# Kernel tuning notes

Measured on AMD Instinct MI355X. Metric: run time of the kernel, lower is better.

The kernel has to match this reference:

```python
import jax, jax.numpy as jnp
import numpy as np

EPS = 1e-5

def _layernorm(x, g, b):
    mu = jnp.mean(x, axis=-1, keepdims=True)
    var = jnp.mean(jnp.square(x - mu), axis=-1, keepdims=True)
    return (x - mu) * jax.lax.rsqrt(var + EPS) * g + b

def setup_inputs() -> dict:
    key = jax.random.key(0)
    ks = jax.random.split(key, 12)
    B, S, D, F = 2, 2048, 1024, 4096
    w = lambda k, shp: jax.random.normal(k, shp, dtype=jnp.float32) * 0.02
    return {
        "x":  jax.random.normal(ks[0], (B, S, D), dtype=jnp.float32),
        "Wq": w(ks[1], (D, D)), "bq": jnp.zeros((D,), jnp.float32),
        "Wk": w(ks[2], (D, D)), "bk": jnp.zeros((D,), jnp.float32),
        "Wv": w(ks[3], (D, D)), "bv": jnp.zeros((D,), jnp.float32),
        "W1": w(ks[4], (F, D)), "b1": jnp.zeros((F,), jnp.float32),
        "W2": w(ks[5], (D, F)), "b2": jnp.zeros((D,), jnp.float32),
        "g1": jnp.ones((D,), jnp.float32), "beta1": jnp.zeros((D,), jnp.float32),
        "g2": jnp.ones((D,), jnp.float32), "beta2": jnp.zeros((D,), jnp.float32),
    }

def reference(x, Wq, bq, Wk, bk, Wv, bv, W1, b1, W2, b2, g1, beta1, g2, beta2):
    B, S, D = x.shape
    H = 16
    dk = D // H
    # QKV projections (torch nn.Linear: y = x @ W.T + b)
    q = (x @ Wq.T + bq).reshape(B, S, H, dk).transpose(0, 2, 1, 3)  # [B,H,S,dk]
    k = (x @ Wk.T + bk).reshape(B, S, H, dk).transpose(0, 2, 1, 3)
    v = (x @ Wv.T + bv).reshape(B, S, H, dk).transpose(0, 2, 1, 3)
    # naive full attention (no mask, dropout=identity in eval)
    scores = jnp.einsum("bhqd,bhkd->bhqk", q, k) / jnp.sqrt(jnp.float32(dk))
    probs = jax.nn.softmax(scores, axis=-1)
    attn = jnp.einsum("bhqk,bhkd->bhqd", probs, v)  # [B,H,S,dk]
    attn_out = attn.transpose(0, 2, 1, 3).reshape(B, S, D)  # NOTE: no output proj (combine unused in source)
    # residual + LN1
    h = _layernorm(x + attn_out, g1, beta1)
    # FFN: linear2(relu(linear1(h)))
    ffn = jax.nn.relu(h @ W1.T + b1) @ W2.T + b2
    # residual + LN2
    return _layernorm(h + ffn, g2, beta2)
```

## Files before the change

kernel.cpp:

```cpp
#include <hip/hip_runtime.h>
#include <stdint.h>

typedef unsigned short u16;
typedef __bf16 bf16x8 __attribute__((ext_vector_type(8)));
typedef short s16x8 __attribute__((ext_vector_type(8)));
typedef float f32x4 __attribute__((ext_vector_type(4)));

union FragU { s16x8 s; bf16x8 b; uint4 u; };

__device__ __forceinline__ f32x4 mfma_bf16(s16x8 a, s16x8 b, f32x4 c) {
    FragU ua, ub; ua.s = a; ub.s = b;
    return __builtin_amdgcn_mfma_f32_16x16x32_bf16(ua.b, ub.b, c, 0, 0, 0);
}

__device__ __forceinline__ u16 f2bf(float f) {
    uint32_t u = __float_as_uint(f);
    u += 0x7fffu + ((u >> 16) & 1u);
    return (u16)(u >> 16);
}

__device__ __forceinline__ float bf2f(u16 u) {
    return __uint_as_float((uint32_t)u << 16);
}

__device__ __forceinline__ void gload_lds16(const void* g, void* l) {
    __builtin_amdgcn_global_load_lds((__attribute__((address_space(1))) void*)g,
                                     (__attribute__((address_space(3))) void*)l,
                                     16, 0, 0);
}

__device__ __forceinline__ void xcd_swz(int& bx, int& by, int& bz) {
    int nx = gridDim.x, ny = gridDim.y;
    int nwg = nx * ny * gridDim.z;
    int lin = blockIdx.x + nx * (blockIdx.y + ny * blockIdx.z);
    int cpx = nwg >> 3;
    int s = (lin & 7) * cpx + (lin >> 3);
    bx = s % nx; s /= nx;
    by = s % ny; bz = s / ny;
}

__global__ void k_cast(const float* __restrict__ in, u16* __restrict__ out, int n4) {
    int i = blockIdx.x * blockDim.x + threadIdx.x;
    int stride = gridDim.x * blockDim.x;
    for (; i < n4; i += stride) {
        float4 v = ((const float4*)in)[i];
        u16 us[4] = {f2bf(v.x), f2bf(v.y), f2bf(v.z), f2bf(v.w)};
        *(uint2*)(out + (size_t)i * 4) = *(uint2*)us;
    }
}

template<int RELU, int OUTMODE>
__device__ __forceinline__ void gemm_body(
    u16* __restrict__ As, u16* __restrict__ Bs,
    const u16* __restrict__ A, const u16* __restrict__ W,
    const float* __restrict__ bias, void* __restrict__ Cout,
    int M, int N, int K, int row0, int col0, int kbeg, int kend)
{
    const int tid  = threadIdx.x;
    const int wid  = tid >> 6;
    const int lane = tid & 63;
    const int g    = lane >> 4;
    const int cc   = lane & 15;
    const int wr   = wid >> 1;
    const int wc   = wid & 1;

    f32x4 zero = {0.f, 0.f, 0.f, 0.f};
    f32x4 acc[4][4];
#pragma unroll
    for (int i = 0; i < 4; i++)
#pragma unroll
        for (int j = 0; j < 4; j++) acc[i][j] = zero;

    const int srow = tid >> 3;
    const int scol = ((tid & 7) ^ (srow & 7)) * 8;
    const u16* gA0 = A + (size_t)(row0 + srow) * K + scol;
    const u16* gB0 = W + (size_t)(col0 + srow) * K + scol;
    u16* lA0 = &As[wid * 512];
    u16* lB0 = &Bs[wid * 512];

    const int xm = (cc & 7);

    for (int k0 = kbeg; k0 < kend; k0 += 64) {
#pragma unroll
        for (int j = 0; j < 4; j++)
            gload_lds16(gA0 + (size_t)(j * 32) * K + k0, lA0 + j * 2048);
#pragma unroll
        for (int j = 0; j < 4; j++)
            gload_lds16(gB0 + (size_t)(j * 32) * K + k0, lB0 + j * 2048);
        __syncthreads();

#pragma unroll
        for (int h = 0; h < 2; h++) {
            const int slot = ((h * 4 + g) ^ xm) * 8;
            s16x8 af[4], bf[4];
#pragma unroll
            for (int mi = 0; mi < 4; mi++)
                af[mi] = *(const s16x8*)&As[(wr * 64 + mi * 16 + cc) * 64 + slot];
#pragma unroll
            for (int ni = 0; ni < 4; ni++)
                bf[ni] = *(const s16x8*)&Bs[(wc * 64 + ni * 16 + cc) * 64 + slot];
#pragma unroll
            for (int mi = 0; mi < 4; mi++)
#pragma unroll
                for (int ni = 0; ni < 4; ni++)
                    acc[mi][ni] = mfma_bf16(af[mi], bf[ni], acc[mi][ni]);
        }
        __syncthreads();
    }

#pragma unroll
    for (int ni = 0; ni < 4; ni++) {
        int col = col0 + wc * 64 + ni * 16 + cc;
        float bvv = 0.f;
        if (OUTMODE != 2) bvv = bias[col];
        if (OUTMODE == 3) {
            int head = col >> 6, dh = col & 63;
#pragma unroll
            for (int mi = 0; mi < 4; mi++) {
                int row = row0 + wr * 64 + mi * 16 + g * 4;
                int bb = row >> 11, sl = row & 2047;
                u16 us[4];
#pragma unroll
                for (int r = 0; r < 4; r++) us[r] = f2bf(acc[mi][ni][r] + bvv);
                *(uint2*)&((u16*)Cout)[(((size_t)(bb * 16 + head) * 64 + dh) << 11) + sl]
                    = *(uint2*)us;
            }
        } else {
#pragma unroll
            for (int mi = 0; mi < 4; mi++) {
                int row = row0 + wr * 64 + mi * 16 + g * 4;
#pragma unroll
                for (int r = 0; r < 4; r++) {
                    float v = acc[mi][ni][r] + bvv;
                    if (RELU) v = fmaxf(v, 0.f);
                    size_t idx = (size_t)(row + r) * N + col;
                    if (OUTMODE == 0) ((float*)Cout)[idx] = v;
                    else              ((u16*)Cout)[idx] = f2bf(v);
                }
            }
        }
    }
}

#define GEMM_LDS_DECL \
    __shared__ __align__(16) u16 As[128 * 64]; \
    __shared__ __align__(16) u16 Bs[128 * 64];

__global__ __launch_bounds__(256, 4) void k_gemm_qkv(
    const u16* __restrict__ A, const u16* __restrict__ Wq, const u16* __restrict__ Wk,
    const u16* __restrict__ Wv, const float* __restrict__ bq, const float* __restrict__ bk,
    const float* __restrict__ bv, u16* __restrict__ Q, u16* __restrict__ K,
    u16* __restrict__ Vt, int M, int N, int Kd)
{
    GEMM_LDS_DECL
    int bx, by, bz; xcd_swz(bx, by, bz);
    if (bz == 0)
        gemm_body<0, 1>(As, Bs, A, Wq, bq, Q,  M, N, Kd, by * 128, bx * 128, 0, Kd);
    else if (bz == 1)
        gemm_body<0, 1>(As, Bs, A, Wk, bk, K,  M, N, Kd, by * 128, bx * 128, 0, Kd);
    else
        gemm_body<0, 3>(As, Bs, A, Wv, bv, Vt, M, N, Kd, by * 128, bx * 128, 0, Kd);
}

__global__ __launch_bounds__(256, 4) void k_gemm_relu_bf16(
    const u16* __restrict__ A, const u16* __restrict__ W, const float* __restrict__ bias,
    u16* __restrict__ C, int M, int N, int K)
{
    GEMM_LDS_DECL
    int bx, by, bz; xcd_swz(bx, by, bz);
    gemm_body<1, 1>(As, Bs, A, W, bias, C, M, N, K, by * 128, bx * 128, 0, K);
}

__global__ __launch_bounds__(256, 4) void k_gemm_part(
    const u16* __restrict__ A, const u16* __restrict__ W,
    u16* __restrict__ p0, u16* __restrict__ p1, u16* __restrict__ p2, u16* __restrict__ p3,
    int M, int N, int K)
{
    GEMM_LDS_DECL
    int bx, by, bz; xcd_swz(bx, by, bz);
    u16* out = (bz == 0) ? p0 : (bz == 1) ? p1 : (bz == 2) ? p2 : p3;
    gemm_body<0, 2>(As, Bs, A, W, nullptr, out, M, N, K, by * 128, bx * 128, bz * 1024, bz * 1024 + 1024);
}

__global__ __launch_bounds__(512, 4) void k_flash(
    const u16* __restrict__ Q, const u16* __restrict__ Kb,
    const u16* __restrict__ Vt, float* __restrict__ O)
{
    constexpr int S = 2048, Dm = 1024, H = 16;
    constexpr int KVB = 128, NT = S / KVB;
    constexpr float qsc = 0.125f * 1.44269504f;
    int bx, by, bz; xcd_swz(bx, by, bz);
    int qt = bx, h = by, b = bz;
    int tid = threadIdx.x, wid = tid >> 6, lane = tid & 63;
    int g = lane >> 4, cc = lane & 15;

    __shared__ __align__(16) u16 Ks[2][128 * 64];
    __shared__ __align__(16) u16 Vs[64 * 128];

    int q0 = qt * 128 + wid * 16;
    size_t base = (size_t)b * S * Dm + h * 64;

    FragU uq0, uq1, qs0, qs1;
    uq0.s = *(const s16x8*)(Q + base + (size_t)(q0 + cc) * Dm + g * 8);
    uq1.s = *(const s16x8*)(Q + base + (size_t)(q0 + cc) * Dm + 32 + g * 8);
#pragma unroll
    for (int e = 0; e < 8; e++) {
        qs0.b[e] = (__bf16)((float)uq0.b[e] * qsc);
        qs1.b[e] = (__bf16)((float)uq1.b[e] * qsc);
    }
    s16x8 qf0 = qs0.s, qf1 = qs1.s;

    f32x4 minit = {-8.f, -8.f, -8.f, -8.f};
    f32x4 zero = {0.f, 0.f, 0.f, 0.f};
    f32x4 o[4];
#pragma unroll
    for (int t = 0; t < 4; t++) o[t] = zero;
    f32x4 lacc = zero;

    const int krow = tid >> 3;
    const int kcol = ((tid & 7) ^ (krow & 7)) * 8;
    const u16* kSrcBase = Kb + base + (size_t)krow * Dm + kcol;
    const int kOff = wid * 512;

    const int vrow = tid >> 3;
    const int vch  = (tid & 7) * 8;
    const int xmv  = (vrow & 7) << 3;
    const int cb0  = ((vch >> 5) << 5) | (((vch >> 4) & 1) << 2) | (((vch >> 2) & 3) << 3);
    const int cb1  = cb0 + 64;
    const u16* vSrcBase = Vt + (size_t)(b * H + h) * 64 * S + (size_t)vrow * S;
    u16* vq0a = &Vs[(vrow * 128 + cb0) ^ xmv];
    u16* vq0b = &Vs[(vrow * 128 + cb0 + 8) ^ xmv];
    u16* vq1a = &Vs[(vrow * 128 + cb1) ^ xmv];
    u16* vq1b = &Vs[(vrow * 128 + cb1 + 8) ^ xmv];

    const int xm = cc & 7;

    gload_lds16(kSrcBase,                   &Ks[0][kOff]);
    gload_lds16(kSrcBase + (size_t)64 * Dm, &Ks[0][kOff + 4096]);
    __builtin_amdgcn_sched_barrier(0);
    s16x8 vpre0 = *(const s16x8*)(vSrcBase + vch);
    s16x8 vpre1 = *(const s16x8*)(vSrcBase + 64 + vch);
    __builtin_amdgcn_sched_barrier(0);

    for (int it = 0; it < NT; ++it) {
        const int cur = it & 1;
        const int kv0 = it * KVB;

        asm volatile("s_waitcnt vmcnt(2)" ::: "memory");
        __builtin_amdgcn_s_barrier();
        __builtin_amdgcn_sched_barrier(0);

        {
            FragU a0, a1; a0.s = vpre0; a1.s = vpre1;
            *(uint2*)vq0a = make_uint2(a0.u.x, a0.u.y);
            *(uint2*)vq0b = make_uint2(a0.u.z, a0.u.w);
            *(uint2*)vq1a = make_uint2(a1.u.x, a1.u.y);
            *(uint2*)vq1b = make_uint2(a1.u.z, a1.u.w);
        }
        __builtin_amdgcn_sched_barrier(0);
        if (it + 1 < NT) {
            gload_lds16(kSrcBase + (size_t)(kv0 + KVB) * Dm,      &Ks[cur ^ 1][kOff]);
            gload_lds16(kSrcBase + (size_t)(kv0 + KVB + 64) * Dm, &Ks[cur ^ 1][kOff + 4096]);
        }
        __builtin_amdgcn_sched_barrier(0);
        asm volatile("s_waitcnt lgkmcnt(0)" ::: "memory");
        __builtin_amdgcn_s_barrier();
        __builtin_amdgcn_sched_barrier(0);

        const u16* Kc = Ks[cur];
        f32x4 sacc[8];
#pragma unroll
        for (int t = 0; t < 8; t++) sacc[t] = minit;
        __builtin_amdgcn_s_setprio(1);
#pragma unroll
        for (int t = 0; t < 8; t++) {
            const u16* kr = &Kc[(t * 16 + cc) * 64];
            s16x8 kf0 = *(const s16x8*)(kr + ((0 + g) ^ xm) * 8);
            s16x8 kf1 = *(const s16x8*)(kr + ((4 + g) ^ xm) * 8);
            sacc[t] = mfma_bf16(kf0, qf0, sacc[t]);
            sacc[t] = mfma_bf16(kf1, qf1, sacc[t]);
        }
        __builtin_amdgcn_s_setprio(0);

        FragU pb[4];
#pragma unroll
        for (int t = 0; t < 8; t++)
#pragma unroll
            for (int r = 0; r < 4; r++) {
                float pv = __builtin_amdgcn_exp2f(sacc[t][r]);
                lacc[r] += pv;
                pb[t >> 1].b[(t & 1) * 4 + r] = (__bf16)pv;
            }

        __builtin_amdgcn_s_setprio(1);
#pragma unroll
        for (int td = 0; td < 4; td++) {
            const int rb = (td * 16 + cc) * 128;
#pragma unroll
            for (int kk = 0; kk < 4; kk++) {
                s16x8 vf = *(const s16x8*)&Vs[(rb + kk * 32 + g * 8) ^ (xm << 3)];
                o[td] = mfma_bf16(vf, pb[kk].s, o[td]);
            }
        }
        __builtin_amdgcn_s_setprio(0);

        if (it + 1 < NT) {
            vpre0 = *(const s16x8*)(vSrcBase + kv0 + KVB + vch);
            vpre1 = *(const s16x8*)(vSrcBase + kv0 + KVB + 64 + vch);
        }
        __builtin_amdgcn_sched_barrier(0);
    }

    float l_run = (lacc[0] + lacc[1]) + (lacc[2] + lacc[3]);
    l_run += __shfl_xor(l_run, 16, 64);
    l_run += __shfl_xor(l_run, 32, 64);
    float inv = 1.f / l_run;
#pragma unroll
    for (int td = 0; td < 4; td++) {
        float4 st = {o[td][0] * inv, o[td][1] * inv, o[td][2] * inv, o[td][3] * inv};
        *(float4*)&O[(size_t)(b * S + q0 + cc) * Dm + h * 64 + td * 16 + g * 4] = st;
    }
}

__global__ __launch_bounds__(256) void k_ln1(
    const float* __restrict__ A, const float* __restrict__ B,
    const float* __restrict__ gw, const float* __restrict__ bw,
    u16* __restrict__ outb)
{
    constexpr int D = 1024;
    int row = blockIdx.x;
    int t = threadIdx.x;
    int lane = t & 63, wid = t >> 6;
    float4 va = ((const float4*)(A + (size_t)row * D))[t];
    float4 vb = ((const float4*)(B + (size_t)row * D))[t];
    float v0 = va.x + vb.x, v1 = va.y + vb.y, v2 = va.z + vb.z, v3 = va.w + vb.w;
    float sum = v0 + v1 + v2 + v3;
    float sq  = v0 * v0 + v1 * v1 + v2 * v2 + v3 * v3;
#pragma unroll
    for (int off = 1; off < 64; off <<= 1) {
        sum += __shfl_xor(sum, off, 64);
        sq  += __shfl_xor(sq,  off, 64);
    }
    __shared__ float s1[4], s2[4];
    if (lane == 0) { s1[wid] = sum; s2[wid] = sq; }
    __syncthreads();
    sum = s1[0] + s1[1] + s1[2] + s1[3];
    sq  = s2[0] + s2[1] + s2[2] + s2[3];
    float mu  = sum * (1.f / D);
    float var = sq * (1.f / D) - mu * mu;
    float rs  = rsqrtf(var + 1e-5f);
    float4 gv = ((const float4*)gw)[t];
    float4 bv = ((const float4*)bw)[t];
    u16 us[4] = {f2bf((v0 - mu) * rs * gv.x + bv.x),
                 f2bf((v1 - mu) * rs * gv.y + bv.y),
                 f2bf((v2 - mu) * rs * gv.z + bv.z),
                 f2bf((v3 - mu) * rs * gv.w + bv.w)};
    *(uint2*)(outb + (size_t)row * D + t * 4) = *(uint2*)us;
}

__global__ __launch_bounds__(256) void k_ln2(
    const u16* __restrict__ A,
    const u16* __restrict__ p0, const u16* __restrict__ p1,
    const u16* __restrict__ p2, const u16* __restrict__ p3,
    const float* __restrict__ bias,
    const float* __restrict__ gw, const float* __restrict__ bw,
    float* __restrict__ outf)
{
    constexpr int D = 1024;
    int row = blockIdx.x;
    int t = threadIdx.x;
    int lane = t & 63, wid = t >> 6;
    size_t idx = (size_t)row * D + t * 4;
    uint2 ha = *(const uint2*)(A + idx);
    float4 bb = ((const float4*)bias)[t];
    float v0 = bf2f((u16)ha.x)         + bb.x;
    float v1 = bf2f((u16)(ha.x >> 16)) + bb.y;
    float v2 = bf2f((u16)ha.y)         + bb.z;
    float v3 = bf2f((u16)(ha.y >> 16)) + bb.w;
    const u16* ps[4] = {p0, p1, p2, p3};
#pragma unroll
    for (int pi = 0; pi < 4; pi++) {
        uint2 q = *(const uint2*)(ps[pi] + idx);
        v0 += bf2f((u16)q.x);
        v1 += bf2f((u16)(q.x >> 16));
        v2 += bf2f((u16)q.y);
        v3 += bf2f((u16)(q.y >> 16));
    }
    float sum = v0 + v1 + v2 + v3;
    float sq  = v0 * v0 + v1 * v1 + v2 * v2 + v3 * v3;
#pragma unroll
    for (int off = 1; off < 64; off <<= 1) {
        sum += __shfl_xor(sum, off, 64);
        sq  += __shfl_xor(sq,  off, 64);
    }
    __shared__ float s1[4], s2[4];
    if (lane == 0) { s1[wid] = sum; s2[wid] = sq; }
    __syncthreads();
    sum = s1[0] + s1[1] + s1[2] + s1[3];
    sq  = s2[0] + s2[1] + s2[2] + s2[3];
    float mu  = sum * (1.f / D);
    float var = sq * (1.f / D) - mu * mu;
    float rs  = rsqrtf(var + 1e-5f);
    float4 gv = ((const float4*)gw)[t];
    float4 bv = ((const float4*)bw)[t];
    float4 yo = {(v0 - mu) * rs * gv.x + bv.x,
                 (v1 - mu) * rs * gv.y + bv.y,
                 (v2 - mu) * rs * gv.z + bv.z,
                 (v3 - mu) * rs * gv.w + bv.w};
    ((float4*)(outf + (size_t)row * D))[t] = yo;
}

extern "C" void kernel_launch(void* const* d_in, const int* in_sizes, int n_in,
                              void* d_out, int out_size, void* d_ws, size_t ws_size,
                              hipStream_t stream)
{
    constexpr int B = 2, S = 2048, D = 1024, F = 4096, H = 16;
    constexpr int M = B * S;
    const float* x   = (const float*)d_in[0];
    const float* Wq  = (const float*)d_in[1];
    const float* bq  = (const float*)d_in[2];
    const float* Wk  = (const float*)d_in[3];
    const float* bk  = (const float*)d_in[4];
    const float* Wv  = (const float*)d_in[5];
    const float* bv  = (const float*)d_in[6];
    const float* W1  = (const float*)d_in[7];
    const float* b1  = (const float*)d_in[8];
    const float* W2  = (const float*)d_in[9];
    const float* b2  = (const float*)d_in[10];
    const float* g1  = (const float*)d_in[11];
    const float* be1 = (const float*)d_in[12];
    const float* g2  = (const float*)d_in[13];
    const float* be2 = (const float*)d_in[14];
    float* out = (float*)d_out;

    char* ws = (char*)d_ws;
    size_t off = 0;
    auto alloc = [&](size_t bytes) {
        void* p = ws + off;
        off += (bytes + 255) & ~(size_t)255;
        return p;
    };
    u16* xb   = (u16*)alloc((size_t)M * D * 2);
    u16* wqb  = (u16*)alloc((size_t)D * D * 2);
    u16* wkb  = (u16*)alloc((size_t)D * D * 2);
    u16* wvb  = (u16*)alloc((size_t)D * D * 2);
    u16* w1b  = (u16*)alloc((size_t)F * D * 2);
    u16* w2b  = (u16*)alloc((size_t)D * F * 2);
    u16* Qb   = (u16*)alloc((size_t)M * D * 2);
    u16* Kbf  = (u16*)alloc((size_t)M * D * 2);
    u16* Vtb  = (u16*)alloc((size_t)M * D * 2);
    u16* ffn1 = (u16*)alloc((size_t)M * F * 2);
    float* attn = (float*)alloc((size_t)M * D * 4);
    u16* hb     = (u16*)alloc((size_t)M * D * 2);
    u16* p0 = xb;
    u16* p1 = w1b;
    u16* p2 = (u16*)attn;
    u16* p3 = ((u16*)attn) + (size_t)M * D;

    dim3 blk(256);
    k_cast<<<dim3(512), blk, 0, stream>>>(x,  xb,  M * D / 4);
    k_cast<<<dim3(256), blk, 0, stream>>>(Wq, wqb, D * D / 4);
    k_cast<<<dim3(256), blk, 0, stream>>>(Wk, wkb, D * D / 4);
    k_cast<<<dim3(256), blk, 0, stream>>>(Wv, wvb, D * D / 4);
    k_cast<<<dim3(512), blk, 0, stream>>>(W1, w1b, F * D / 4);
    k_cast<<<dim3(512), blk, 0, stream>>>(W2, w2b, D * F / 4);

    k_gemm_qkv<<<dim3(D / 128, M / 128, 3), blk, 0, stream>>>(
        xb, wqb, wkb, wvb, bq, bk, bv, Qb, Kbf, Vtb, M, D, D);
    k_flash<<<dim3(S / 128, H, B), dim3(512), 0, stream>>>(Qb, Kbf, Vtb, attn);
    k_ln1<<<dim3(M), blk, 0, stream>>>(x, attn, g1, be1, hb);
    k_gemm_relu_bf16<<<dim3(F / 128, M / 128), blk, 0, stream>>>(hb, w1b, b1, ffn1, M, F, D);
    k_gemm_part<<<dim3(D / 128, M / 128, 4), blk, 0, stream>>>(
        ffn1, w2b, p0, p1, p2, p3, M, D, F);
    k_ln2<<<dim3(M), blk, 0, stream>>>(hb, p0, p1, p2, p3, b2, g2, be2, out);
}
```

Measured before the change: 197.2 us.

## Process two query tiles per wave in flash attention with 256-thread blocks

The flash attention kernel now uses 4 waves per block, each handling 32 query rows as two 16-row sub-tiles. Each K and V fragment read from LDS feeds two MFMAs, which halves LDS fragment traffic per unit of work. K and V tile loads are redistributed so each thread loads twice as much. In exchange, accumulator and register pressure roughly doubles and there are fewer waves per block to hide latency.

```diff
diff --git a/kernel.cpp b/kernel.cpp
--- a/kernel.cpp
+++ b/kernel.cpp
@@ -182,7 +182,7 @@
     gemm_body<0, 2>(As, Bs, A, W, nullptr, out, M, N, K, by * 128, bx * 128, bz * 1024, bz * 1024 + 1024);
 }
 
-__global__ __launch_bounds__(512, 4) void k_flash(
+__global__ __launch_bounds__(256, 2) void k_flash(
     const u16* __restrict__ Q, const u16* __restrict__ Kb,
     const u16* __restrict__ Vt, float* __restrict__ O)
 {
@@ -197,70 +197,89 @@
     __shared__ __align__(16) u16 Ks[2][128 * 64];
     __shared__ __align__(16) u16 Vs[64 * 128];
 
-    int q0 = qt * 128 + wid * 16;
+    int q0 = qt * 128 + wid * 32;
     size_t base = (size_t)b * S * Dm + h * 64;
 
-    FragU uq0, uq1, qs0, qs1;
-    uq0.s = *(const s16x8*)(Q + base + (size_t)(q0 + cc) * Dm + g * 8);
-    uq1.s = *(const s16x8*)(Q + base + (size_t)(q0 + cc) * Dm + 32 + g * 8);
+    FragU t0, t1, t2, t3, qa0, qa1, qb0, qb1;
+    t0.s = *(const s16x8*)(Q + base + (size_t)(q0 + cc) * Dm + g * 8);
+    t1.s = *(const s16x8*)(Q + base + (size_t)(q0 + cc) * Dm + 32 + g * 8);
+    t2.s = *(const s16x8*)(Q + base + (size_t)(q0 + 16 + cc) * Dm + g * 8);
+    t3.s = *(const s16x8*)(Q + base + (size_t)(q0 + 16 + cc) * Dm + 32 + g * 8);
 #pragma unroll
     for (int e = 0; e < 8; e++) {
-        qs0.b[e] = (__bf16)((float)uq0.b[e] * qsc);
-        qs1.b[e] = (__bf16)((float)uq1.b[e] * qsc);
-    }
-    s16x8 qf0 = qs0.s, qf1 = qs1.s;
+        qa0.b[e] = (__bf16)((float)t0.b[e] * qsc);
+        qa1.b[e] = (__bf16)((float)t1.b[e] * qsc);
+        qb0.b[e] = (__bf16)((float)t2.b[e] * qsc);
+        qb1.b[e] = (__bf16)((float)t3.b[e] * qsc);
+    }
 
     f32x4 minit = {-8.f, -8.f, -8.f, -8.f};
     f32x4 zero = {0.f, 0.f, 0.f, 0.f};
-    f32x4 o[4];
-#pragma unroll
-    for (int t = 0; t < 4; t++) o[t] = zero;
-    f32x4 lacc = zero;
-
-    const int krow = tid >> 3;
-    const int kcol = ((tid & 7) ^ (krow & 7)) * 8;
-    const u16* kSrcBase = Kb + base + (size_t)krow * Dm + kcol;
+    f32x4 o0[4], o1[4];
+#pragma unroll
+    for (int t = 0; t < 4; t++) { o0[t] = zero; o1[t] = zero; }
+    f32x4 la0 = zero, la1 = zero;
+
+    const int srow = tid >> 3;
+    const int kcol = ((tid & 7) ^ (srow & 7)) * 8;
+    const u16* kSrcBase = Kb + base + (size_t)srow * Dm + kcol;
     const int kOff = wid * 512;
 
-    const int vrow = tid >> 3;
-    const int vch  = (tid & 7) * 8;
+    const int vrow = tid >> 2;
+    const int vchb = (tid & 3) * 32;
     const int xmv  = (vrow & 7) << 3;
-    const int cb0  = ((vch >> 5) << 5) | (((vch >> 4) & 1) << 2) | (((vch >> 2) & 3) << 3);
-    const int cb1  = cb0 + 64;
-    const u16* vSrcBase = Vt + (size_t)(b * H + h) * 64 * S + (size_t)vrow * S;
-    u16* vq0a = &Vs[(vrow * 128 + cb0) ^ xmv];
-    u16* vq0b = &Vs[(vrow * 128 + cb0 + 8) ^ xmv];
-    u16* vq1a = &Vs[(vrow * 128 + cb1) ^ xmv];
-    u16* vq1b = &Vs[(vrow * 128 + cb1 + 8) ^ xmv];
+    int vo0, vo1, vo2, vo3;
+    {
+        int s0 = vchb, s1 = vchb + 8, s2 = vchb + 16, s3 = vchb + 24;
+        int c0 = ((s0 >> 5) << 5) | (((s0 >> 4) & 1) << 2) | (((s0 >> 2) & 3) << 3);
+        int c1 = ((s1 >> 5) << 5) | (((s1 >> 4) & 1) << 2) | (((s1 >> 2) & 3) << 3);
+        int c2 = ((s2 >> 5) << 5) | (((s2 >> 4) & 1) << 2) | (((s2 >> 2) & 3) << 3);
+        int c3 = ((s3 >> 5) << 5) | (((s3 >> 4) & 1) << 2) | (((s3 >> 2) & 3) << 3);
+        vo0 = (vrow * 128 + c0) ^ xmv;
+        vo1 = (vrow * 128 + c1) ^ xmv;
+        vo2 = (vrow * 128 + c2) ^ xmv;
+        vo3 = (vrow * 128 + c3) ^ xmv;
+    }
+    const u16* vSrcBase = Vt + (size_t)(b * H + h) * 64 * S + (size_t)vrow * S + vchb;
 
     const int xm = cc & 7;
 
-    gload_lds16(kSrcBase,                   &Ks[0][kOff]);
-    gload_lds16(kSrcBase + (size_t)64 * Dm, &Ks[0][kOff + 4096]);
+#pragma unroll
+    for (int j = 0; j < 4; j++)
+        gload_lds16(kSrcBase + (size_t)(j * 32) * Dm, &Ks[0][j * 2048 + kOff]);
     __builtin_amdgcn_sched_barrier(0);
-    s16x8 vpre0 = *(const s16x8*)(vSrcBase + vch);
-    s16x8 vpre1 = *(const s16x8*)(vSrcBase + 64 + vch);
+    s16x8 vp0 = *(const s16x8*)(vSrcBase);
+    s16x8 vp1 = *(const s16x8*)(vSrcBase + 8);
+    s16x8 vp2 = *(const s16x8*)(vSrcBase + 16);
+    s16x8 vp3 = *(const s16x8*)(vSrcBase + 24);
     __builtin_amdgcn_sched_barrier(0);
 
     for (int it = 0; it < NT; ++it) {
         const int cur = it & 1;
         const int kv0 = it * KVB;
 
-        asm volatile("s_waitcnt vmcnt(2)" ::: "memory");
+        asm volatile("s_waitcnt vmcnt(4)" ::: "memory");
         __builtin_amdgcn_s_barrier();
         __builtin_amdgcn_sched_barrier(0);
 
         {
-            FragU a0, a1; a0.s = vpre0; a1.s = vpre1;
-            *(uint2*)vq0a = make_uint2(a0.u.x, a0.u.y);
-            *(uint2*)vq0b = make_uint2(a0.u.z, a0.u.w);
-            *(uint2*)vq1a = make_uint2(a1.u.x, a1.u.y);
-            *(uint2*)vq1b = make_uint2(a1.u.z, a1.u.w);
+            FragU a0, a1, a2, a3;
+            a0.s = vp0; a1.s = vp1; a2.s = vp2; a3.s = vp3;
+            *(uint2*)&Vs[vo0]     = make_uint2(a0.u.x, a0.u.y);
+            *(uint2*)&Vs[vo0 ^ 8] = make_uint2(a0.u.z, a0.u.w);
+            *(uint2*)&Vs[vo1]     = make_uint2(a1.u.x, a1.u.y);
+            *(uint2*)&Vs[vo1 ^ 8] = make_uint2(a1.u.z, a1.u.w);
+            *(uint2*)&Vs[vo2]     = make_uint2(a2.u.x, a2.u.y);
+            *(uint2*)&Vs[vo2 ^ 8] = make_uint2(a2.u.z, a2.u.w);
+            *(uint2*)&Vs[vo3]     = make_uint2(a3.u.x, a3.u.y);
+            *(uint2*)&Vs[vo3 ^ 8] = make_uint2(a3.u.z, a3.u.w);
         }
         __builtin_amdgcn_sched_barrier(0);
         if (it + 1 < NT) {
-            gload_lds16(kSrcBase + (size_t)(kv0 + KVB) * Dm,      &Ks[cur ^ 1][kOff]);
-            gload_lds16(kSrcBase + (size_t)(kv0 + KVB + 64) * Dm, &Ks[cur ^ 1][kOff + 4096]);
+#pragma unroll
+            for (int j = 0; j < 4; j++)
+                gload_lds16(kSrcBase + (size_t)(kv0 + KVB + j * 32) * Dm,
+                            &Ks[cur ^ 1][j * 2048 + kOff]);
         }
         __builtin_amdgcn_sched_barrier(0);
         asm volatile("s_waitcnt lgkmcnt(0)" ::: "memory");
@@ -268,28 +287,33 @@
         __builtin_amdgcn_sched_barrier(0);
 
         const u16* Kc = Ks[cur];
-        f32x4 sacc[8];
-#pragma unroll
-        for (int t = 0; t < 8; t++) sacc[t] = minit;
+        f32x4 sa[8], sb[8];
+#pragma unroll
+        for (int t = 0; t < 8; t++) { sa[t] = minit; sb[t] = minit; }
         __builtin_amdgcn_s_setprio(1);
 #pragma unroll
         for (int t = 0; t < 8; t++) {
             const u16* kr = &Kc[(t * 16 + cc) * 64];
             s16x8 kf0 = *(const s16x8*)(kr + ((0 + g) ^ xm) * 8);
             s16x8 kf1 = *(const s16x8*)(kr + ((4 + g) ^ xm) * 8);
-            sacc[t] = mfma_bf16(kf0, qf0, sacc[t]);
-            sacc[t] = mfma_bf16(kf1, qf1, sacc[t]);
+            sa[t] = mfma_bf16(kf0, qa0.s, sa[t]);
+            sa[t] = mfma_bf16(kf1, qa1.s, sa[t]);
+            sb[t] = mfma_bf16(kf0, qb0.s, sb[t]);
+            sb[t] = mfma_bf16(kf1, qb1.s, sb[t]);
         }
         __builtin_amdgcn_s_setprio(0);
 
-        FragU pb[4];
+        FragU pa[4], pb[4];
 #pragma unroll
         for (int t = 0; t < 8; t++)
 #pragma unroll
             for (int r = 0; r < 4; r++) {
-                float pv = __builtin_amdgcn_exp2f(sacc[t][r]);
-                lacc[r] += pv;
-                pb[t >> 1].b[(t & 1) * 4 + r] = (__bf16)pv;
+                float pva = __builtin_amdgcn_exp2f(sa[t][r]);
+                float pvb = __builtin_amdgcn_exp2f(sb[t][r]);
+                la0[r] += pva;
+                la1[r] += pvb;
+                pa[t >> 1].b[(t & 1) * 4 + r] = (__bf16)pva;
+                pb[t >> 1].b[(t & 1) * 4 + r] = (__bf16)pvb;
             }
 
         __builtin_amdgcn_s_setprio(1);
@@ -299,26 +323,34 @@
 #pragma unroll
             for (int kk = 0; kk < 4; kk++) {
                 s16x8 vf = *(const s16x8*)&Vs[(rb + kk * 32 + g * 8) ^ (xm << 3)];
-                o[td] = mfma_bf16(vf, pb[kk].s, o[td]);
+                o0[td] = mfma_bf16(vf, pa[kk].s, o0[td]);
+                o1[td] = mfma_bf16(vf, pb[kk].s, o1[td]);
             }
         }
         __builtin_amdgcn_s_setprio(0);
 
         if (it + 1 < NT) {
-            vpre0 = *(const s16x8*)(vSrcBase + kv0 + KVB + vch);
-            vpre1 = *(const s16x8*)(vSrcBase + kv0 + KVB + 64 + vch);
+            vp0 = *(const s16x8*)(vSrcBase + kv0 + KVB);
+            vp1 = *(const s16x8*)(vSrcBase + kv0 + KVB + 8);
+            vp2 = *(const s16x8*)(vSrcBase + kv0 + KVB + 16);
+            vp3 = *(const s16x8*)(vSrcBase + kv0 + KVB + 24);
         }
         __builtin_amdgcn_sched_barrier(0);
     }
 
-    float l_run = (lacc[0] + lacc[1]) + (lacc[2] + lacc[3]);
-    l_run += __shfl_xor(l_run, 16, 64);
-    l_run += __shfl_xor(l_run, 32, 64);
-    float inv = 1.f / l_run;
+    float l0 = (la0[0] + la0[1]) + (la0[2] + la0[3]);
+    float l1 = (la1[0] + la1[1]) + (la1[2] + la1[3]);
+    l0 += __shfl_xor(l0, 16, 64);
+    l0 += __shfl_xor(l0, 32, 64);
+    l1 += __shfl_xor(l1, 16, 64);
+    l1 += __shfl_xor(l1, 32, 64);
+    float i0 = 1.f / l0, i1 = 1.f / l1;
 #pragma unroll
     for (int td = 0; td < 4; td++) {
-        float4 st = {o[td][0] * inv, o[td][1] * inv, o[td][2] * inv, o[td][3] * inv};
-        *(float4*)&O[(size_t)(b * S + q0 + cc) * Dm + h * 64 + td * 16 + g * 4] = st;
+        float4 s0 = {o0[td][0] * i0, o0[td][1] * i0, o0[td][2] * i0, o0[td][3] * i0};
+        float4 s1 = {o1[td][0] * i1, o1[td][1] * i1, o1[td][2] * i1, o1[td][3] * i1};
+        *(float4*)&O[(size_t)(b * S + q0 + cc) * Dm + h * 64 + td * 16 + g * 4] = s0;
+        *(float4*)&O[(size_t)(b * S + q0 + 16 + cc) * Dm + h * 64 + td * 16 + g * 4] = s1;
     }
 }
 
@@ -467,7 +499,7 @@
 
     k_gemm_qkv<<<dim3(D / 128, M / 128, 3), blk, 0, stream>>>(
         xb, wqb, wkb, wvb, bq, bk, bv, Qb, Kbf, Vtb, M, D, D);
-    k_flash<<<dim3(S / 128, H, B), dim3(512), 0, stream>>>(Qb, Kbf, Vtb, attn);
+    k_flash<<<dim3(S / 128, H, B), dim3(256), 0, stream>>>(Qb, Kbf, Vtb, attn);
     k_ln1<<<dim3(M), blk, 0, stream>>>(x, attn, g1, be1, hb);
     k_gemm_relu_bf16<<<dim3(F / 128, M / 128), blk, 0, stream>>>(hb, w1b, b1, ffn1, M, F, D);
     k_gemm_part<<<dim3(D / 128, M / 128, 4), blk, 0, stream>>>(
```

Measured after the change: 198.1 us. About the same (+0.4%).
